# Optimization experiments

Measured on AMD Instinct MI355X. Metric: run time of the kernel, lower is better.

The kernel has to match this reference:

```python
import jax, jax.numpy as jnp
import numpy as np
from jax import lax

B, C, H, W = 2, 384, 32, 32
N_HEAD, N_GROUP = 12, 6
HC = C // N_HEAD          # 32 head channels
GC = C // N_GROUP         # 64 group channels
GH = N_HEAD // N_GROUP    # 2 heads per group
KK = 7                    # depthwise kernel (25<=32<=48)
OFF_FACTOR = 2.0
SCALE = HC ** -0.5
EPS = 1e-5


def setup_inputs() -> dict:
    key = jax.random.key(0)
    ks = jax.random.split(key, 16)
    s = 0.02
    inp = {
        "x": jax.random.normal(ks[0], (B, C, H, W), jnp.float32),
        "Wq": jax.random.normal(ks[1], (C, C), jnp.float32) * s,
        "bq": jnp.zeros((C,), jnp.float32),
        "Wk": jax.random.normal(ks[2], (C, C), jnp.float32) * s,
        "bk": jnp.zeros((C,), jnp.float32),
        "Wv": jax.random.normal(ks[3], (C, C), jnp.float32) * s,
        "bv": jnp.zeros((C,), jnp.float32),
        "Wo": jax.random.normal(ks[4], (C, C), jnp.float32) * s,
        "bo": jnp.zeros((C,), jnp.float32),
        "off_dw_w": jax.random.normal(ks[5], (GC, 1, KK, KK), jnp.float32) * s,  # depthwise OIHW
        "off_dw_b": jnp.zeros((GC,), jnp.float32),
        "ln_g": jnp.ones((GC,), jnp.float32),
        "ln_b": jnp.zeros((GC,), jnp.float32),
        "off_pw_w": jax.random.normal(ks[6], (2, GC), jnp.float32) * s,  # 1x1 conv, no bias
        "rpe_table": jax.random.normal(ks[7], (N_HEAD, 2 * H - 1, 2 * W - 1), jnp.float32) * 0.01,
    }
    return inp


def _ref_points(Hk, Wk):
    # torch.linspace(0.5, Hk-0.5, Hk)/Hk*2-1 == ((i+0.5)/Hk)*2-1
    ry = ((jnp.arange(Hk, dtype=jnp.float32) + 0.5) / Hk) * 2.0 - 1.0
    rx = ((jnp.arange(Wk, dtype=jnp.float32) + 0.5) / Wk) * 2.0 - 1.0
    gy, gx = jnp.meshgrid(ry, rx, indexing='ij')
    return jnp.stack((gy, gx), axis=-1)  # [Hk, Wk, 2] in (y, x) order


def _grid_sample(img, grid):
    # img: [N, Cc, Hi, Wi]; grid: [N, Hg, Wg, 2] in (x, y), align_corners=True, zeros padding
    N, Cc, Hi, Wi = img.shape
    Hg, Wg = grid.shape[1], grid.shape[2]
    gx = (grid[..., 0] + 1.0) * 0.5 * (Wi - 1)
    gy = (grid[..., 1] + 1.0) * 0.5 * (Hi - 1)
    x0 = jnp.floor(gx)
    y0 = jnp.floor(gy)
    wx = gx - x0
    wy = gy - y0
    img_f = img.reshape(N, Cc, Hi * Wi)

    def corner(xi, yi, w):
        valid = (xi >= 0) & (xi <= Wi - 1) & (yi >= 0) & (yi <= Hi - 1)
        xc = jnp.clip(xi, 0, Wi - 1).astype(jnp.int32)
        yc = jnp.clip(yi, 0, Hi - 1).astype(jnp.int32)
        idx = (yc * Wi + xc).reshape(N, 1, Hg * Wg)
        vals = jnp.take_along_axis(img_f, jnp.broadcast_to(idx, (N, Cc, Hg * Wg)), axis=2)
        w = (w * valid.astype(img.dtype)).reshape(N, 1, Hg * Wg)
        return vals * w

    out = (corner(x0, y0, (1 - wx) * (1 - wy))
           + corner(x0 + 1, y0, wx * (1 - wy))
           + corner(x0, y0 + 1, (1 - wx) * wy)
           + corner(x0 + 1, y0 + 1, wx * wy))
    return out.reshape(N, Cc, Hg, Wg)


def _conv1x1(x, w, b=None):
    y = jnp.einsum('bchw,oc->bohw', x, w)
    if b is not None:
        y = y + b[None, :, None, None]
    return y


def _forward(x, Wq, bq, Wk, bk, Wv, bv, Wo, bo, off_dw_w, off_dw_b, ln_g, ln_b, off_pw_w, rpe_table):
    q = _conv1x1(x, Wq, bq)                                        # [B, C, H, W]
    q_off = q.reshape(B * N_GROUP, GC, H, W)
    # conv_offset: depthwise conv -> LayerNorm(ch) -> GELU -> 1x1 conv to 2 ch
    o = lax.conv_general_dilated(q_off, off_dw_w, (1, 1), ((KK // 2, KK // 2), (KK // 2, KK // 2)),
                                 feature_group_count=GC,
                                 dimension_numbers=('NCHW', 'OIHW', 'NCHW'))
    o = o + off_dw_b[None, :, None, None]
    mu = jnp.mean(o, axis=1, keepdims=True)
    var = jnp.mean((o - mu) ** 2, axis=1, keepdims=True)
    o = (o - mu) * lax.rsqrt(var + EPS) * ln_g[None, :, None, None] + ln_b[None, :, None, None]
    o = jax.nn.gelu(o, approximate=False)
    off = jnp.einsum('bchw,oc->bohw', o, off_pw_w)                 # [BG, 2, Hs, Ws]
    Hs, Ws = off.shape[2], off.shape[3]
    n_sample = Hs * Ws
    off_range = jnp.array([1.0 / Hs, 1.0 / Ws], jnp.float32).reshape(1, 2, 1, 1)
    off = jnp.tanh(off) * off_range * OFF_FACTOR
    off = jnp.transpose(off, (0, 2, 3, 1))                         # [BG, Hs, Ws, 2] (y, x)
    pos = off + _ref_points(Hs, Ws)[None]                          # [BG, Hs, Ws, 2]

    x_g = x.reshape(B * N_GROUP, GC, H, W)
    x_s = _grid_sample(x_g, pos[..., ::-1])                        # [BG, GC, Hs, Ws]
    x_s = x_s.reshape(B, C, 1, n_sample)

    k = _conv1x1(x_s, Wk, bk).reshape(B * N_HEAD, HC, n_sample)
    v = _conv1x1(x_s, Wv, bv).reshape(B * N_HEAD, HC, n_sample)
    qh = q.reshape(B * N_HEAD, HC, H * W)
    attn = jnp.einsum('bcm,bcn->bmn', qh, k) * SCALE               # [BH, HW, ns]

    # RPE: bilinear lookup of relative-position table at query-sample displacements
    q_grid = _ref_points(H, W).reshape(1, H * W, 1, 2)
    disp = (q_grid - pos.reshape(B * N_GROUP, 1, n_sample, 2)) * 0.5  # [BG, HW, ns, 2] (y, x)
    rpe_b = jnp.broadcast_to(rpe_table[None], (B, N_HEAD, 2 * H - 1, 2 * W - 1))
    rpe_b = rpe_b.reshape(B * N_GROUP, GH, 2 * H - 1, 2 * W - 1)
    attn_bias = _grid_sample(rpe_b, disp[..., ::-1])               # [BG, GH, HW, ns]
    attn = attn + attn_bias.reshape(B * N_HEAD, H * W, n_sample)

    attn = jax.nn.softmax(attn, axis=2)
    out = jnp.einsum('bmn,bcn->bcm', attn, v).reshape(B, C, H, W)
    y = _conv1x1(out, Wo, bo)
    return y


def reference(x, Wq, bq, Wk, bk, Wv, bv, Wo, bo, off_dw_w, off_dw_b, ln_g, ln_b, off_pw_w, rpe_table):
    return _forward(x, Wq, bq, Wk, bk, Wv, bv, Wo, bo,
                    off_dw_w, off_dw_b, ln_g, ln_b, off_pw_w, rpe_table)
```

## Files before the change

kernel.cpp:

```cpp
#include <hip/hip_runtime.h>
#include <hip/hip_fp16.h>
#include <math.h>

#define HH 32
#define WW 32
#define HWSZ 1024
#define CC 384
#define NHEAD 12
#define NGROUP 6
#define HC 32
#define GC 64
#define NS 1024
#define ATTN_SCALE 0.17677669529663687f

typedef _Float16 half8_t __attribute__((ext_vector_type(8)));
typedef _Float16 half4_t __attribute__((ext_vector_type(4)));
typedef _Float16 half2_t __attribute__((ext_vector_type(2)));
typedef float    f4_t    __attribute__((ext_vector_type(4)));

template<int XLO>
__global__ __launch_bounds__(256) void gemm_wx(
    const float* __restrict__ W, const float* __restrict__ bias,
    const float* __restrict__ X, float* __restrict__ Y)
{
    const int bz = blockIdx.z;
    const int tm = blockIdx.y * 32;
    const int tn = blockIdx.x * 64;
    const int tid = threadIdx.x;
    const int w = tid >> 6, lane = tid & 63;
    const int quad = lane >> 4, lcol = lane & 15;

    __shared__ _Float16 sWh[32][40];
    __shared__ _Float16 sXh[64][40];
    __shared__ _Float16 sXl[XLO ? 64 : 1][40];

    const float* Xb = X + (size_t)bz * CC * 1024;
    float* Yb = Y + (size_t)bz * CC * 1024;

    f4_t acc0 = {0.f, 0.f, 0.f, 0.f}, acc1 = {0.f, 0.f, 0.f, 0.f};

    for (int k0 = 0; k0 < CC; k0 += 32) {
        {
            int m = tid >> 3, k4 = (tid & 7) * 4;
            float4 wv = *(const float4*)&W[(size_t)(tm + m) * CC + k0 + k4];
            half4_t h; h[0] = (_Float16)wv.x; h[1] = (_Float16)wv.y;
            h[2] = (_Float16)wv.z; h[3] = (_Float16)wv.w;
            *(half4_t*)&sWh[m][k4] = h;
        }
        {
            int k = tid >> 3, nj = tid & 7;
            const float* xr = &Xb[(size_t)(k0 + k) * 1024 + tn + nj];
#pragma unroll
            for (int i = 0; i < 8; ++i) {
                float v = xr[8 * i];
                _Float16 h = (_Float16)v;
                sXh[nj + 8 * i][k] = h;
                if (XLO) sXl[nj + 8 * i][k] = (_Float16)(v - (float)h);
            }
        }
        __syncthreads();

        half8_t Ah0 = *(const half8_t*)&sWh[lcol][quad * 8];
        half8_t Ah1 = *(const half8_t*)&sWh[16 + lcol][quad * 8];
        half8_t Bh  = *(const half8_t*)&sXh[w * 16 + lcol][quad * 8];
        acc0 = __builtin_amdgcn_mfma_f32_16x16x32_f16(Ah0, Bh, acc0, 0, 0, 0);
        acc1 = __builtin_amdgcn_mfma_f32_16x16x32_f16(Ah1, Bh, acc1, 0, 0, 0);
        if (XLO) {
            half8_t Bl = *(const half8_t*)&sXl[w * 16 + lcol][quad * 8];
            acc0 = __builtin_amdgcn_mfma_f32_16x16x32_f16(Ah0, Bl, acc0, 0, 0, 0);
            acc1 = __builtin_amdgcn_mfma_f32_16x16x32_f16(Ah1, Bl, acc1, 0, 0, 0);
        }
        __syncthreads();
    }

#pragma unroll
    for (int r = 0; r < 4; ++r) {
        int m0 = tm + quad * 4 + r;
        Yb[(size_t)m0 * 1024 + tn + w * 16 + lcol]        = acc0[r] + bias[m0];
        Yb[(size_t)(m0 + 16) * 1024 + tn + w * 16 + lcol] = acc1[r] + bias[m0 + 16];
    }
}

__global__ __launch_bounds__(256) void gemm_kv_f16(
    const float* __restrict__ Wk, const float* __restrict__ bk,
    const float* __restrict__ Wv, const float* __restrict__ bv,
    const float* __restrict__ X,
    _Float16* __restrict__ khT, _Float16* __restrict__ vhb)
{
    const int bz = blockIdx.z >> 1, which = blockIdx.z & 1;
    const int head = blockIdx.y;
    const int tm = head * 32;
    const int tn = blockIdx.x * 64;
    const int tid = threadIdx.x;
    const int w = tid >> 6, lane = tid & 63;
    const int quad = lane >> 4, lcol = lane & 15;
    const int bh = bz * 12 + head;

    const float* W    = which ? Wv : Wk;
    const float* bias = which ? bv : bk;

    __shared__ _Float16 sWh[32][40];
    __shared__ _Float16 sXh[64][40];

    const float* Xb = X + (size_t)bz * CC * 1024;

    f4_t acc0 = {0.f, 0.f, 0.f, 0.f}, acc1 = {0.f, 0.f, 0.f, 0.f};

    for (int k0 = 0; k0 < CC; k0 += 32) {
        {
            int m = tid >> 3, k4 = (tid & 7) * 4;
            float4 wv = *(const float4*)&W[(size_t)(tm + m) * CC + k0 + k4];
            half4_t h; h[0] = (_Float16)wv.x; h[1] = (_Float16)wv.y;
            h[2] = (_Float16)wv.z; h[3] = (_Float16)wv.w;
            *(half4_t*)&sWh[m][k4] = h;
        }
        {
            int k = tid >> 3, nj = tid & 7;
            const float* xr = &Xb[(size_t)(k0 + k) * 1024 + tn + nj];
#pragma unroll
            for (int i = 0; i < 8; ++i)
                sXh[nj + 8 * i][k] = (_Float16)xr[8 * i];
        }
        __syncthreads();

        if (which) {
            half8_t Ah0 = *(const half8_t*)&sWh[lcol][quad * 8];
            half8_t Ah1 = *(const half8_t*)&sWh[16 + lcol][quad * 8];
            half8_t Bh  = *(const half8_t*)&sXh[w * 16 + lcol][quad * 8];
            acc0 = __builtin_amdgcn_mfma_f32_16x16x32_f16(Ah0, Bh, acc0, 0, 0, 0);
            acc1 = __builtin_amdgcn_mfma_f32_16x16x32_f16(Ah1, Bh, acc1, 0, 0, 0);
        } else {
            half8_t Ah  = *(const half8_t*)&sXh[w * 16 + lcol][quad * 8];
            half8_t Bh0 = *(const half8_t*)&sWh[lcol][quad * 8];
            half8_t Bh1 = *(const half8_t*)&sWh[16 + lcol][quad * 8];
            acc0 = __builtin_amdgcn_mfma_f32_16x16x32_f16(Ah, Bh0, acc0, 0, 0, 0);
            acc1 = __builtin_amdgcn_mfma_f32_16x16x32_f16(Ah, Bh1, acc1, 0, 0, 0);
        }
        __syncthreads();
    }

    if (which) {
#pragma unroll
        for (int r = 0; r < 4; ++r) {
            int hc0 = quad * 4 + r;
            vhb[((size_t)bh * 32 + hc0) * 1024 + tn + w * 16 + lcol] =
                (_Float16)(acc0[r] + bias[tm + hc0]);
            vhb[((size_t)bh * 32 + hc0 + 16) * 1024 + tn + w * 16 + lcol] =
                (_Float16)(acc1[r] + bias[tm + hc0 + 16]);
        }
    } else {
        float bk0 = bias[tm + lcol], bk1 = bias[tm + 16 + lcol];
#pragma unroll
        for (int r = 0; r < 4; ++r) {
            int n = tn + w * 16 + quad * 4 + r;
            khT[((size_t)bh * 1024 + n) * 32 + lcol]      = (_Float16)(acc0[r] + bk0);
            khT[((size_t)bh * 1024 + n) * 32 + 16 + lcol] = (_Float16)(acc1[r] + bk1);
        }
    }
}

__global__ __launch_bounds__(256) void dwconv_kernel(
    const float* __restrict__ q, const float* __restrict__ dww,
    const float* __restrict__ dwb, float* __restrict__ oconv)
{
    const int bc = blockIdx.x;
    const int bg = bc >> 6, c = bc & 63;
    const int b = bg / 6, g = bg % 6;
    const float* plane = q + ((size_t)b * CC + g * 64 + c) * 1024;

    __shared__ float sp[1024];
    __shared__ float sw[49];
    const int tid = threadIdx.x;
    for (int i = tid; i < 1024; i += 256) sp[i] = plane[i];
    if (tid < 49) sw[tid] = dww[c * 49 + tid];
    __syncthreads();

    const float bias = dwb[c];
    for (int i = tid; i < 1024; i += 256) {
        int y = i >> 5, x = i & 31;
        float s = 0.f;
#pragma unroll
        for (int ky = 0; ky < 7; ++ky) {
            int yy = y + ky - 3;
            if (yy < 0 || yy > 31) continue;
#pragma unroll
            for (int kx = 0; kx < 7; ++kx) {
                int xx = x + kx - 3;
                if (xx < 0 || xx > 31) continue;
                s += sp[yy * 32 + xx] * sw[ky * 7 + kx];
            }
        }
        oconv[(size_t)bc * 1024 + i] = s + bias;
    }
}

__global__ __launch_bounds__(256) void offset_sample_kernel(
    const float* __restrict__ oconv, const float* __restrict__ lng,
    const float* __restrict__ lnb, const float* __restrict__ pw,
    const float* __restrict__ x, float* __restrict__ pos,
    float* __restrict__ xs)
{
    const int bg = blockIdx.y;
    const int px0 = blockIdx.x * 64;
    const int t = threadIdx.x;
    const int cg = t >> 6, pl = t & 63;
    const int px = px0 + pl;
    const int b = bg / 6, g = bg % 6;

    __shared__ float red[4][64];
    __shared__ float spos[64][2];

    const float* base = oconv + ((size_t)bg * 64 + cg * 16) * 1024 + px;
    float col[16];
    float s = 0.f;
#pragma unroll
    for (int i = 0; i < 16; ++i) { col[i] = base[(size_t)i * 1024]; s += col[i]; }
    red[cg][pl] = s;
    __syncthreads();
    float mu = (red[0][pl] + red[1][pl] + red[2][pl] + red[3][pl]) * (1.f / 64.f);
    float v = 0.f;
#pragma unroll
    for (int i = 0; i < 16; ++i) { float d = col[i] - mu; v += d * d; }
    __syncthreads();
    red[cg][pl] = v;
    __syncthreads();
    float inv = rsqrtf((red[0][pl] + red[1][pl] + red[2][pl] + red[3][pl]) * (1.f / 64.f) + 1e-5f);

    float oy = 0.f, ox = 0.f;
#pragma unroll
    for (int i = 0; i < 16; ++i) {
        int c = cg * 16 + i;
        float val = (col[i] - mu) * inv * lng[c] + lnb[c];
        float gl = 0.5f * val * (1.f + erff(val * 0.70710678118654752440f));
        oy += gl * pw[c];
        ox += gl * pw[64 + c];
    }
    __syncthreads();
    red[cg][pl] = oy;
    __syncthreads();
    float oyt = red[0][pl] + red[1][pl] + red[2][pl] + red[3][pl];
    __syncthreads();
    red[cg][pl] = ox;
    __syncthreads();
    if (cg == 0) {
        float oxt = red[0][pl] + red[1][pl] + red[2][pl] + red[3][pl];
        float offy = tanhf(oyt) * (2.0f / 32.0f);
        float offx = tanhf(oxt) * (2.0f / 32.0f);
        int y = px >> 5, xx = px & 31;
        float ry = ((y + 0.5f) / 32.f) * 2.f - 1.f;
        float rx = ((xx + 0.5f) / 32.f) * 2.f - 1.f;
        float py = offy + ry, pxv = offx + rx;
        spos[pl][0] = py; spos[pl][1] = pxv;
        pos[((size_t)bg * 1024 + px) * 2 + 0] = py;
        pos[((size_t)bg * 1024 + px) * 2 + 1] = pxv;
    }
    __syncthreads();

    float py = spos[pl][0], pxv = spos[pl][1];
    float gx = (pxv + 1.f) * 0.5f * 31.f;
    float gy = (py + 1.f) * 0.5f * 31.f;
    float x0f = floorf(gx), y0f = floorf(gy);
    float wx = gx - x0f, wy = gy - y0f;
    int x0 = (int)x0f, y0 = (int)y0f;
    float vx0 = ((unsigned)x0 <= 31u) ? 1.f : 0.f;
    float vx1 = ((unsigned)(x0 + 1) <= 31u) ? 1.f : 0.f;
    float vy0 = ((unsigned)y0 <= 31u) ? 1.f : 0.f;
    float vy1 = ((unsigned)(y0 + 1) <= 31u) ? 1.f : 0.f;
    float w00 = (1.f - wx) * (1.f - wy) * vx0 * vy0;
    float w01 = wx * (1.f - wy) * vx1 * vy0;
    float w10 = (1.f - wx) * wy * vx0 * vy1;
    float w11 = wx * wy * vx1 * vy1;
    int xc0 = min(max(x0, 0), 31), xc1 = min(max(x0 + 1, 0), 31);
    int yc0 = min(max(y0, 0), 31), yc1 = min(max(y0 + 1, 0), 31);
    int i00 = yc0 * 32 + xc0, i01 = yc0 * 32 + xc1;
    int i10 = yc1 * 32 + xc0, i11 = yc1 * 32 + xc1;

    const float* xb = x + ((size_t)b * CC + g * 64 + cg * 16) * 1024;
    float* xso = xs + ((size_t)b * CC + g * 64 + cg * 16) * 1024 + px;
#pragma unroll
    for (int i = 0; i < 16; ++i) {
        const float* plane = xb + (size_t)i * 1024;
        xso[(size_t)i * 1024] = plane[i00] * w00 + plane[i01] * w01
                              + plane[i10] * w10 + plane[i11] * w11;
    }
}

__global__ __launch_bounds__(256) void attn_mfma_kernel(
    const float* __restrict__ q, const _Float16* __restrict__ khT,
    const _Float16* __restrict__ vhb, const float* __restrict__ pos,
    const float* __restrict__ rpe, float* __restrict__ out)
{
    const int bh = blockIdx.y;
    const int b = bh / 12, head = bh % 12;
    const int bg = b * 6 + (head >> 1);
    const int mblk = blockIdx.x * 16;
    const int tid = threadIdx.x;
    const int w = tid >> 6, lane = tid & 63;
    const int quad = lane >> 4, lcol = lane & 15;

    __shared__ __align__(16) char smem[19584];
    half2_t*  srpe2 = (half2_t*)smem;
    _Float16* sqh   = (_Float16*)(smem + 8832);
    _Float16* spw   = (_Float16*)(smem + 9856) + w * (16 * 72);
    float*    cml   = (float*)(smem + 19072);
    float*    comb  = (float*)(smem + 9856);

    const float qyw = (((mblk >> 5) + 0.5f) * (1.f / 32.f)) * 2.f - 1.f;
    int r0; {
        float gy_lo = (qyw - 1.03125f) * 15.5f + 31.f;
        r0 = (int)floorf(gy_lo);
        r0 = min(max(r0, 0), 28);
    }

    const float* rp = rpe + (size_t)head * 3969;
    for (int i = tid; i < 35 * 63; i += 256) {
        int y = i / 63, xx = i - y * 63;
        int gi = (r0 + y) * 63 + xx;
        float v0 = rp[gi];
        float v1 = (xx < 62) ? rp[gi + 1] : 0.f;
        half2_t hv; hv[0] = (_Float16)v0; hv[1] = (_Float16)v1;
        srpe2[i] = hv;
    }
    {
        const float* qb = q + ((size_t)b * CC + head * 32) * 1024 + mblk;
        for (int i = tid; i < 512; i += 256) {
            int hc = i >> 4, m = i & 15;
            sqh[m * 32 + hc] = (_Float16)qb[(size_t)hc * 1024 + m];
        }
    }
    __syncthreads();

    half8_t qf = *(const half8_t*)&sqh[lcol * 32 + quad * 8];

    const float qx = (((mblk & 31) + lcol + 0.5f) * (1.f / 32.f)) * 2.f - 1.f;

    const float2* pgv = (const float2*)(pos + (size_t)bg * 2048);
    const _Float16* khb = khT + (size_t)bh * 1024 * 32;
    const _Float16* vhh = vhb + (size_t)bh * 32 * 1024;

    f4_t o0 = {0.f, 0.f, 0.f, 0.f}, o1 = {0.f, 0.f, 0.f, 0.f};
    float mrun = -3.0e38f, lrun = 0.f;

#pragma unroll 1
    for (int c = 0; c < 4; ++c) {
        const int n0 = w * 256 + c * 64;
        f4_t S[4];
#pragma unroll
        for (int t = 0; t < 4; ++t) {
            half8_t kh = *(const half8_t*)&khb[(size_t)(n0 + t * 16 + lcol) * 32 + quad * 8];
            f4_t s = {0.f, 0.f, 0.f, 0.f};
            s = __builtin_amdgcn_mfma_f32_16x16x32_f16(kh, qf, s, 0, 0, 0);
#pragma unroll
            for (int r = 0; r < 4; ++r) {
                int key = n0 + t * 16 + quad * 4 + r;
                float2 pp = pgv[key];
                float gy = (qyw - pp.x) * 15.5f + 31.f;
                float gx = (qx  - pp.y) * 15.5f + 31.f;
                float y0f = floorf(gy), x0f = floorf(gx);
                float wy = gy - y0f, wx = gx - x0f;
                int i00 = ((int)y0f - r0) * 63 + (int)x0f;
                half2_t p0 = srpe2[i00];
                half2_t p1 = srpe2[i00 + 63];
                float r00 = (float)p0[0], r01 = (float)p0[1];
                float r10 = (float)p1[0], r11 = (float)p1[1];
                float top = r00 + (r01 - r00) * wx;
                float bot = r10 + (r11 - r10) * wx;
                s[r] = s[r] * ATTN_SCALE + top + (bot - top) * wy;
            }
            S[t] = s;
        }

        float cm = -3.0e38f;
#pragma unroll
        for (int t = 0; t < 4; ++t)
            cm = fmaxf(cm, fmaxf(fmaxf(S[t][0], S[t][1]), fmaxf(S[t][2], S[t][3])));
        cm = fmaxf(cm, __shfl_xor(cm, 16));
        cm = fmaxf(cm, __shfl_xor(cm, 32));
        float mnew = fmaxf(mrun, cm);
        float alpha = __expf(mrun - mnew);
        mrun = mnew;

        float rs = 0.f;
#pragma unroll
        for (int t = 0; t < 4; ++t) {
            float p0 = __expf(S[t][0] - mnew);
            float p1 = __expf(S[t][1] - mnew);
            float p2 = __expf(S[t][2] - mnew);
            float p3 = __expf(S[t][3] - mnew);
            rs += (p0 + p1) + (p2 + p3);
            half4_t h;
            h[0] = (_Float16)p0; h[1] = (_Float16)p1;
            h[2] = (_Float16)p2; h[3] = (_Float16)p3;
            *(half4_t*)&spw[lcol * 72 + t * 16 + quad * 4] = h;
        }
        rs += __shfl_xor(rs, 16);
        rs += __shfl_xor(rs, 32);
        lrun = lrun * alpha + rs;
        o0 *= alpha; o1 *= alpha;

#pragma unroll
        for (int kp = 0; kp < 2; ++kp) {
            half8_t pb = *(const half8_t*)&spw[lcol * 72 + kp * 32 + quad * 8];
            int nb = n0 + kp * 32 + quad * 8;
            half8_t v0 = *(const half8_t*)&vhh[(size_t)lcol * 1024 + nb];
            half8_t v1 = *(const half8_t*)&vhh[(size_t)(16 + lcol) * 1024 + nb];
            o0 = __builtin_amdgcn_mfma_f32_16x16x32_f16(v0, pb, o0, 0, 0, 0);
            o1 = __builtin_amdgcn_mfma_f32_16x16x32_f16(v1, pb, o1, 0, 0, 0);
        }
    }

    __syncthreads();

    *(f4_t*)&comb[(w * 16 + lcol) * 36 + quad * 4]      = o0;
    *(f4_t*)&comb[(w * 16 + lcol) * 36 + 16 + quad * 4] = o1;
    if (quad == 0) {
        cml[(w * 16 + lcol) * 2]     = mrun;
        cml[(w * 16 + lcol) * 2 + 1] = lrun;
    }
    __syncthreads();

#pragma unroll
    for (int i = 0; i < 2; ++i) {
        int idx = tid + i * 256;
        int qq = idx >> 5, hc = idx & 31;
        float m0 = cml[(0 * 16 + qq) * 2], l0 = cml[(0 * 16 + qq) * 2 + 1];
        float m1 = cml[(1 * 16 + qq) * 2], l1 = cml[(1 * 16 + qq) * 2 + 1];
        float m2 = cml[(2 * 16 + qq) * 2], l2 = cml[(2 * 16 + qq) * 2 + 1];
        float m3 = cml[(3 * 16 + qq) * 2], l3 = cml[(3 * 16 + qq) * 2 + 1];
        float ms = fmaxf(fmaxf(m0, m1), fmaxf(m2, m3));
        float e0 = __expf(m0 - ms), e1 = __expf(m1 - ms);
        float e2 = __expf(m2 - ms), e3 = __expf(m3 - ms);
        float L = e0 * l0 + e1 * l1 + e2 * l2 + e3 * l3;
        float o = e0 * comb[(0 * 16 + qq) * 36 + hc]
                + e1 * comb[(1 * 16 + qq) * 36 + hc]
                + e2 * comb[(2 * 16 + qq) * 36 + hc]
                + e3 * comb[(3 * 16 + qq) * 36 + hc];
        out[((size_t)b * CC + head * 32 + hc) * 1024 + mblk + qq] = o / L;
    }
}

extern "C" void kernel_launch(void* const* d_in, const int* in_sizes, int n_in,
                              void* d_out, int out_size, void* d_ws, size_t ws_size,
                              hipStream_t stream) {
    const float* x   = (const float*)d_in[0];
    const float* Wq  = (const float*)d_in[1];
    const float* bq  = (const float*)d_in[2];
    const float* Wk  = (const float*)d_in[3];
    const float* bk  = (const float*)d_in[4];
    const float* Wv  = (const float*)d_in[5];
    const float* bv  = (const float*)d_in[6];
    const float* Wo  = (const float*)d_in[7];
    const float* bo  = (const float*)d_in[8];
    const float* dww = (const float*)d_in[9];
    const float* dwb = (const float*)d_in[10];
    const float* lng = (const float*)d_in[11];
    const float* lnb = (const float*)d_in[12];
    const float* pw  = (const float*)d_in[13];
    const float* rpe = (const float*)d_in[14];

    float* ws = (float*)d_ws;
    const size_t SZ = 786432;
    float* qbuf  = ws;
    float* xs    = ws + 1 * SZ;
    float* abuf  = ws + 2 * SZ;
    float* oconv = ws + 3 * SZ;
    _Float16* khT = (_Float16*)(ws + 4 * SZ);
    _Float16* vhb = (_Float16*)(ws + 5 * SZ);
    float* pos   = ws + 6 * SZ;

    dim3 gqo(16, 12, 2);
    gemm_wx<0><<<gqo, 256, 0, stream>>>(Wq, bq, x, qbuf);
    dwconv_kernel<<<768, 256, 0, stream>>>(qbuf, dww, dwb, oconv);
    offset_sample_kernel<<<dim3(16, 12), 256, 0, stream>>>(oconv, lng, lnb, pw, x, pos, xs);
    gemm_kv_f16<<<dim3(16, 12, 4), 256, 0, stream>>>(Wk, bk, Wv, bv, xs, khT, vhb);
    attn_mfma_kernel<<<dim3(64, 24), 256, 0, stream>>>(qbuf, khT, vhb, pos, rpe, abuf);
    gemm_wx<1><<<gqo, 256, 0, stream>>>(Wo, bo, abuf, (float*)d_out);
}
```

Baseline: 179.5 us.

## Fuse K/V projections, split offset sampling over channels, prefetch K/V in attention

```diff
diff --git a/kernel.cpp b/kernel.cpp
--- a/kernel.cpp
+++ b/kernel.cpp
@@ -81,13 +81,13 @@
     }
 }
 
-__global__ __launch_bounds__(256) void gemm_kv_f16(
+__global__ __launch_bounds__(256) void gemm_kv_fused(
     const float* __restrict__ Wk, const float* __restrict__ bk,
     const float* __restrict__ Wv, const float* __restrict__ bv,
     const float* __restrict__ X,
     _Float16* __restrict__ khT, _Float16* __restrict__ vhb)
 {
-    const int bz = blockIdx.z >> 1, which = blockIdx.z & 1;
+    const int bz = blockIdx.z;
     const int head = blockIdx.y;
     const int tm = head * 32;
     const int tn = blockIdx.x * 64;
@@ -96,23 +96,25 @@
     const int quad = lane >> 4, lcol = lane & 15;
     const int bh = bz * 12 + head;
 
-    const float* W    = which ? Wv : Wk;
-    const float* bias = which ? bv : bk;
-
-    __shared__ _Float16 sWh[32][40];
+    __shared__ _Float16 sWk[32][40], sWv[32][40];
     __shared__ _Float16 sXh[64][40];
 
     const float* Xb = X + (size_t)bz * CC * 1024;
 
-    f4_t acc0 = {0.f, 0.f, 0.f, 0.f}, acc1 = {0.f, 0.f, 0.f, 0.f};
+    f4_t ak0 = {0.f, 0.f, 0.f, 0.f}, ak1 = {0.f, 0.f, 0.f, 0.f};
+    f4_t av0 = {0.f, 0.f, 0.f, 0.f}, av1 = {0.f, 0.f, 0.f, 0.f};
 
     for (int k0 = 0; k0 < CC; k0 += 32) {
         {
             int m = tid >> 3, k4 = (tid & 7) * 4;
-            float4 wv = *(const float4*)&W[(size_t)(tm + m) * CC + k0 + k4];
-            half4_t h; h[0] = (_Float16)wv.x; h[1] = (_Float16)wv.y;
-            h[2] = (_Float16)wv.z; h[3] = (_Float16)wv.w;
-            *(half4_t*)&sWh[m][k4] = h;
+            float4 wk = *(const float4*)&Wk[(size_t)(tm + m) * CC + k0 + k4];
+            float4 wv = *(const float4*)&Wv[(size_t)(tm + m) * CC + k0 + k4];
+            half4_t hk; hk[0] = (_Float16)wk.x; hk[1] = (_Float16)wk.y;
+            hk[2] = (_Float16)wk.z; hk[3] = (_Float16)wk.w;
+            half4_t hv; hv[0] = (_Float16)wv.x; hv[1] = (_Float16)wv.y;
+            hv[2] = (_Float16)wv.z; hv[3] = (_Float16)wv.w;
+            *(half4_t*)&sWk[m][k4] = hk;
+            *(half4_t*)&sWv[m][k4] = hv;
         }
         {
             int k = tid >> 3, nj = tid & 7;
@@ -123,38 +125,35 @@
         }
         __syncthreads();
 
-        if (which) {
-            half8_t Ah0 = *(const half8_t*)&sWh[lcol][quad * 8];
-            half8_t Ah1 = *(const half8_t*)&sWh[16 + lcol][quad * 8];
-            half8_t Bh  = *(const half8_t*)&sXh[w * 16 + lcol][quad * 8];
-            acc0 = __builtin_amdgcn_mfma_f32_16x16x32_f16(Ah0, Bh, acc0, 0, 0, 0);
-            acc1 = __builtin_amdgcn_mfma_f32_16x16x32_f16(Ah1, Bh, acc1, 0, 0, 0);
-        } else {
-            half8_t Ah  = *(const half8_t*)&sXh[w * 16 + lcol][quad * 8];
-            half8_t Bh0 = *(const half8_t*)&sWh[lcol][quad * 8];
-            half8_t Bh1 = *(const half8_t*)&sWh[16 + lcol][quad * 8];
-            acc0 = __builtin_amdgcn_mfma_f32_16x16x32_f16(Ah, Bh0, acc0, 0, 0, 0);
-            acc1 = __builtin_amdgcn_mfma_f32_16x16x32_f16(Ah, Bh1, acc1, 0, 0, 0);
-        }
+        half8_t Xa = *(const half8_t*)&sXh[w * 16 + lcol][quad * 8];
+        half8_t K0 = *(const half8_t*)&sWk[lcol][quad * 8];
+        half8_t K1 = *(const half8_t*)&sWk[16 + lcol][quad * 8];
+        half8_t V0 = *(const half8_t*)&sWv[lcol][quad * 8];
+        half8_t V1 = *(const half8_t*)&sWv[16 + lcol][quad * 8];
+        ak0 = __builtin_amdgcn_mfma_f32_16x16x32_f16(Xa, K0, ak0, 0, 0, 0);
+        ak1 = __builtin_amdgcn_mfma_f32_16x16x32_f16(Xa, K1, ak1, 0, 0, 0);
+        av0 = __builtin_amdgcn_mfma_f32_16x16x32_f16(V0, Xa, av0, 0, 0, 0);
+        av1 = __builtin_amdgcn_mfma_f32_16x16x32_f16(V1, Xa, av1, 0, 0, 0);
         __syncthreads();
     }
 
-    if (which) {
+    {
+        float bk0 = bk[tm + lcol], bk1 = bk[tm + 16 + lcol];
+#pragma unroll
+        for (int r = 0; r < 4; ++r) {
+            int n = tn + w * 16 + quad * 4 + r;
+            khT[((size_t)bh * 1024 + n) * 32 + lcol]      = (_Float16)(ak0[r] + bk0);
+            khT[((size_t)bh * 1024 + n) * 32 + 16 + lcol] = (_Float16)(ak1[r] + bk1);
+        }
+    }
+    {
 #pragma unroll
         for (int r = 0; r < 4; ++r) {
             int hc0 = quad * 4 + r;
             vhb[((size_t)bh * 32 + hc0) * 1024 + tn + w * 16 + lcol] =
-                (_Float16)(acc0[r] + bias[tm + hc0]);
+                (_Float16)(av0[r] + bv[tm + hc0]);
             vhb[((size_t)bh * 32 + hc0 + 16) * 1024 + tn + w * 16 + lcol] =
-                (_Float16)(acc1[r] + bias[tm + hc0 + 16]);
-        }
-    } else {
-        float bk0 = bias[tm + lcol], bk1 = bias[tm + 16 + lcol];
-#pragma unroll
-        for (int r = 0; r < 4; ++r) {
-            int n = tn + w * 16 + quad * 4 + r;
-            khT[((size_t)bh * 1024 + n) * 32 + lcol]      = (_Float16)(acc0[r] + bk0);
-            khT[((size_t)bh * 1024 + n) * 32 + 16 + lcol] = (_Float16)(acc1[r] + bk1);
+                (_Float16)(av1[r] + bv[tm + hc0 + 16]);
         }
     }
 }
@@ -201,6 +200,7 @@
     float* __restrict__ xs)
 {
     const int bg = blockIdx.y;
+    const int cs = blockIdx.z;
     const int px0 = blockIdx.x * 64;
     const int t = threadIdx.x;
     const int cg = t >> 6, pl = t & 63;
@@ -251,8 +251,10 @@
         float rx = ((xx + 0.5f) / 32.f) * 2.f - 1.f;
         float py = offy + ry, pxv = offx + rx;
         spos[pl][0] = py; spos[pl][1] = pxv;
-        pos[((size_t)bg * 1024 + px) * 2 + 0] = py;
-        pos[((size_t)bg * 1024 + px) * 2 + 1] = pxv;
+        if (cs == 0) {
+            pos[((size_t)bg * 1024 + px) * 2 + 0] = py;
+            pos[((size_t)bg * 1024 + px) * 2 + 1] = pxv;
+        }
     }
     __syncthreads();
 
@@ -275,10 +277,11 @@
     int i00 = yc0 * 32 + xc0, i01 = yc0 * 32 + xc1;
     int i10 = yc1 * 32 + xc0, i11 = yc1 * 32 + xc1;
 
-    const float* xb = x + ((size_t)b * CC + g * 64 + cg * 16) * 1024;
-    float* xso = xs + ((size_t)b * CC + g * 64 + cg * 16) * 1024 + px;
-#pragma unroll
-    for (int i = 0; i < 16; ++i) {
+    const int c0 = cs * 16 + cg * 4;
+    const float* xb = x + ((size_t)b * CC + g * 64 + c0) * 1024;
+    float* xso = xs + ((size_t)b * CC + g * 64 + c0) * 1024 + px;
+#pragma unroll
+    for (int i = 0; i < 4; ++i) {
         const float* plane = xb + (size_t)i * 1024;
         xso[(size_t)i * 1024] = plane[i00] * w00 + plane[i01] * w01
                               + plane[i10] * w10 + plane[i11] * w11;
@@ -331,7 +334,6 @@
     __syncthreads();
 
     half8_t qf = *(const half8_t*)&sqh[lcol * 32 + quad * 8];
-
     const float qx = (((mblk & 31) + lcol + 0.5f) * (1.f / 32.f)) * 2.f - 1.f;
 
     const float2* pgv = (const float2*)(pos + (size_t)bg * 2048);
@@ -344,12 +346,24 @@
 #pragma unroll 1
     for (int c = 0; c < 4; ++c) {
         const int n0 = w * 256 + c * 64;
+
+        half8_t khv[4];
+#pragma unroll
+        for (int t = 0; t < 4; ++t)
+            khv[t] = *(const half8_t*)&khb[(size_t)(n0 + t * 16 + lcol) * 32 + quad * 8];
+        half8_t vv0[2], vv1[2];
+#pragma unroll
+        for (int kp = 0; kp < 2; ++kp) {
+            int nb = n0 + kp * 32 + quad * 8;
+            vv0[kp] = *(const half8_t*)&vhh[(size_t)lcol * 1024 + nb];
+            vv1[kp] = *(const half8_t*)&vhh[(size_t)(16 + lcol) * 1024 + nb];
+        }
+
         f4_t S[4];
 #pragma unroll
         for (int t = 0; t < 4; ++t) {
-            half8_t kh = *(const half8_t*)&khb[(size_t)(n0 + t * 16 + lcol) * 32 + quad * 8];
             f4_t s = {0.f, 0.f, 0.f, 0.f};
-            s = __builtin_amdgcn_mfma_f32_16x16x32_f16(kh, qf, s, 0, 0, 0);
+            s = __builtin_amdgcn_mfma_f32_16x16x32_f16(khv[t], qf, s, 0, 0, 0);
 #pragma unroll
             for (int r = 0; r < 4; ++r) {
                 int key = n0 + t * 16 + quad * 4 + r;
@@ -401,11 +415,8 @@
 #pragma unroll
         for (int kp = 0; kp < 2; ++kp) {
             half8_t pb = *(const half8_t*)&spw[lcol * 72 + kp * 32 + quad * 8];
-            int nb = n0 + kp * 32 + quad * 8;
-            half8_t v0 = *(const half8_t*)&vhh[(size_t)lcol * 1024 + nb];
-            half8_t v1 = *(const half8_t*)&vhh[(size_t)(16 + lcol) * 1024 + nb];
-            o0 = __builtin_amdgcn_mfma_f32_16x16x32_f16(v0, pb, o0, 0, 0, 0);
-            o1 = __builtin_amdgcn_mfma_f32_16x16x32_f16(v1, pb, o1, 0, 0, 0);
+            o0 = __builtin_amdgcn_mfma_f32_16x16x32_f16(vv0[kp], pb, o0, 0, 0, 0);
+            o1 = __builtin_amdgcn_mfma_f32_16x16x32_f16(vv1[kp], pb, o1, 0, 0, 0);
         }
     }
 
@@ -471,8 +482,8 @@
     dim3 gqo(16, 12, 2);
     gemm_wx<0><<<gqo, 256, 0, stream>>>(Wq, bq, x, qbuf);
     dwconv_kernel<<<768, 256, 0, stream>>>(qbuf, dww, dwb, oconv);
-    offset_sample_kernel<<<dim3(16, 12), 256, 0, stream>>>(oconv, lng, lnb, pw, x, pos, xs);
-    gemm_kv_f16<<<dim3(16, 12, 4), 256, 0, stream>>>(Wk, bk, Wv, bv, xs, khT, vhb);
+    offset_sample_kernel<<<dim3(16, 12, 4), 256, 0, stream>>>(oconv, lng, lnb, pw, x, pos, xs);
+    gemm_kv_fused<<<dim3(16, 12, 2), 256, 0, stream>>>(Wk, bk, Wv, bv, xs, khT, vhb);
     attn_mfma_kernel<<<dim3(64, 24), 256, 0, stream>>>(qbuf, khT, vhb, pos, rpe, abuf);
     gemm_wx<1><<<gqo, 256, 0, stream>>>(Wo, bo, abuf, (float*)d_out);
 }
```

Result: faster. 171.0 us (-4.7%).
